# Optimization experiments

Measured on AMD Instinct MI355X. Metric: run time of the kernel, lower is better.

## Reference

```python
import jax, jax.numpy as jnp
import numpy as np

KSIZE = 5      # equivalent steerable kernel size
KMAX = 3       # max circular harmonic
STRIDE = 2
N_IN, N_OUT = 32, 16
B_TOTAL = 3 + 2 * KMAX  # 3 radial atoms at k=0, 2 per harmonic k>=1


def _make_basis():
    # Radial steerable base: Gaussian rings x circular harmonics cos(k*theta)/sin(k*theta)
    ys, xs = np.mgrid[:KSIZE, :KSIZE].astype(np.float64) - (KSIZE - 1) / 2
    r = np.sqrt(xs ** 2 + ys ** 2)
    th = np.arctan2(ys, xs)
    ring = lambda r0: np.exp(-(r - r0) ** 2 / (2 * 0.6 ** 2))
    b0 = np.stack([ring(r0) for r0 in (0.0, 1.0, 2.0)])          # (3, 5, 5)
    br, bi = [], []
    for k in range(1, KMAX + 1):
        br.append(np.stack([ring(r0) * np.cos(k * th) for r0 in (1.0, 2.0)]))  # (2,5,5)
        bi.append(np.stack([ring(r0) * np.sin(k * th) for r0 in (1.0, 2.0)]))
    return (b0.astype(np.float32),
            [b.astype(np.float32) for b in br],
            [b.astype(np.float32) for b in bi])


def _conv_transpose(x, w):
    # torch conv_transpose2d (stride=2, padding='same' -> pad=2, output_padding=1)
    # == dilated-input conv with spatially flipped kernel, explicit pad (2,3).
    rhs = jnp.flip(w, axis=(2, 3))  # (o, i, kh, kw)
    return jax.lax.conv_general_dilated(
        x, rhs, window_strides=(1, 1), padding=((2, 3), (2, 3)),
        lhs_dilation=(STRIDE, STRIDE),
        dimension_numbers=('NCHW', 'OIHW', 'NCHW'))


def setup_inputs() -> dict:
    key = jax.random.key(0)
    k1, k2, k3, k4 = jax.random.split(key, 4)
    x = jax.random.normal(k1, (8, N_IN, 192, 192), jnp.float32)
    # alpha[0]=cos-like, alpha[1]=sin-like field at output resolution; not unit-norm,
    # rho is derived from its norm (rho=None path of forward()).
    alpha = jax.random.normal(k2, (2, 8, 1, 384, 384), jnp.float32)
    weights = jax.random.normal(k3, (N_OUT, N_IN, B_TOTAL), jnp.float32) / np.sqrt(N_IN * B_TOTAL)
    bias = jax.random.normal(k4, (N_OUT,), jnp.float32) * 0.05
    return {"x": x, "alpha": alpha, "weights": weights, "bias": bias}


def reference(x, alpha, weights, bias):
    b0, br, bi = _make_basis()
    # normalize_vector: rho = |alpha|, alpha <- alpha / rho
    rho = jnp.sqrt(jnp.sum(alpha * alpha, axis=0))          # (b, 1, Ho, Wo)
    au = alpha / (rho[None] + 1e-8)
    c1, s1 = au[0], au[1]                                    # cos(a), sin(a)
    # k=0 term (rotation invariant)
    out = _conv_transpose(x, jnp.einsum('oib,bhw->oihw', weights[:, :, :3], jnp.asarray(b0)))
    ck, sk = c1, s1
    off = 3
    for k in range(KMAX):  # harmonics k=1..KMAX, steered by cos(k a), sin(k a)
        wk = weights[:, :, off:off + 2]
        off += 2
        Kr = jnp.einsum('oib,bhw->oihw', wk, jnp.asarray(br[k]))
        Ki = jnp.einsum('oib,bhw->oihw', wk, jnp.asarray(bi[k]))
        out = out + _conv_transpose(x, Kr) * ck + _conv_transpose(x, Ki) * sk
        ckn = ck * c1 - sk * s1  # Chebyshev-style recurrence for cos/sin of (k+1)a
        skn = sk * c1 + ck * s1
        ck, sk = ckn, skn
    return rho * out + bias[None, :, None, None]
```

## Files before the change

### kernel.cpp

```cpp
#include <hip/hip_runtime.h>

#define HIN 192
#define WOUT 384
#define NIN 32
#define NOUT 16
#define NSLOT 9
#define HP 194
#define HPLANE (HP * HP)
#define HQBATCH ((size_t)HPLANE * 18)

typedef float v2f __attribute__((ext_vector_type(2)));

__device__ __forceinline__ unsigned short f2bf(float f) {
    union { float f; unsigned int u; } v; v.f = f;
    unsigned int r = v.u + 0x7fffu + ((v.u >> 16) & 1u);
    return (unsigned short)(r >> 16);
}
__device__ __forceinline__ v2f up2(unsigned u) {
    v2f r;
    r.x = __uint_as_float(u << 16);
    r.y = __uint_as_float(u);
    return r;
}

__global__ __launch_bounds__(256) void kprep_w(const float* __restrict__ w, float* __restrict__ Wt) {
    int t = blockIdx.x * 256 + threadIdx.x;
    if (t >= NIN * NSLOT * NOUT) return;
    int c = t >> 8, r = t & 255;
    int i = r >> 3, j = r & 7;
    int m = c * 8 + j;
    int s = m >> 4, o = m & 15;
    Wt[t] = w[(o * NIN + i) * NSLOT + s];
}

__global__ __launch_bounds__(256) void kzero(uint4* __restrict__ hq, int nb) {
    int t = blockIdx.x * 256 + threadIdx.x;
    if (t >= nb * 772) return;
    int b = t / 772, r = t % 772;
    int iy, ix;
    if (r < 194)      { iy = 0;           ix = r; }
    else if (r < 388) { iy = 193;         ix = r - 194; }
    else if (r < 580) { iy = r - 388 + 1; ix = 0; }
    else              { iy = r - 580 + 1; ix = 193; }
    uint4* p = hq + (size_t)b * HQBATCH + iy * HP + ix;
    uint4 z; z.x = 0; z.y = 0; z.z = 0; z.w = 0;
    #pragma unroll
    for (int c = 0; c < 18; ++c) p[(size_t)c * HPLANE] = z;
}

__global__ __launch_bounds__(256) void kA(const float* __restrict__ x,
                                          const float* __restrict__ Wt,
                                          uint4* __restrict__ hq, int n0) {
    const int b = blockIdx.y;
    const int n = n0 + b;
    const int px = blockIdx.x * 256 + threadIdx.x;
    const int iy = px / HIN, ix = px % HIN;
    const float* xp = x + (size_t)n * NIN * HIN * HIN + px;
    float xv[NIN];
    #pragma unroll
    for (int i = 0; i < NIN; ++i) xv[i] = xp[(size_t)i * HIN * HIN];
    const int pos = (iy + 1) * HP + (ix + 1);
    uint4* hb = hq + (size_t)b * HQBATCH;
    #pragma unroll 1
    for (int c = 0; c < 18; ++c) {
        const float* wc = Wt + c * 256;
        float a[8];
        #pragma unroll
        for (int j = 0; j < 8; ++j) a[j] = 0.0f;
        #pragma unroll
        for (int i = 0; i < NIN; ++i) {
            const float xi = xv[i];
            #pragma unroll
            for (int j = 0; j < 8; ++j) a[j] = fmaf(wc[i * 8 + j], xi, a[j]);
        }
        uint4 v;
        v.x = (unsigned)f2bf(a[0]) | ((unsigned)f2bf(a[1]) << 16);
        v.y = (unsigned)f2bf(a[2]) | ((unsigned)f2bf(a[3]) << 16);
        v.z = (unsigned)f2bf(a[4]) | ((unsigned)f2bf(a[5]) << 16);
        v.w = (unsigned)f2bf(a[6]) | ((unsigned)f2bf(a[7]) << 16);
        hb[(size_t)c * HPLANE + pos] = v;
    }
}

__device__ __forceinline__ void angles(const float* __restrict__ alpha, int n, int oy, int ox,
                                       float (&cc)[3], float (&ss)[3], float& rr) {
    const int aoff = (n * WOUT + oy) * WOUT + ox;
    const float a0 = alpha[aoff];
    const float a1 = alpha[(size_t)8 * WOUT * WOUT + aoff];
    rr = sqrtf(a0 * a0 + a1 * a1);
    const float inv = 1.0f / (rr + 1e-8f);
    cc[0] = a0 * inv;                      ss[0] = a1 * inv;
    cc[1] = cc[0] * cc[0] - ss[0] * ss[0]; ss[1] = 2.0f * cc[0] * ss[0];
    cc[2] = cc[1] * cc[0] - ss[1] * ss[0]; ss[2] = ss[1] * cc[0] + cc[1] * ss[0];
}

__device__ __forceinline__ float ebv(const float2 C, int s,
                                     const float (&cc)[3], const float (&ss)[3]) {
    if (s < 3) return C.x;
    if (s < 5) return C.x * cc[0] + C.y * ss[0];
    if (s < 7) return C.x * cc[1] + C.y * ss[1];
    return C.x * cc[2] + C.y * ss[2];
}

template<int PAIR, int HF>
__device__ __forceinline__ void kb_pair(const uint4* __restrict__ hb,
                                        const float* __restrict__ alpha,
                                        const float* __restrict__ bias_,
                                        float (&stage)[2][16][128],
                                        const float2 (&Cb)[NSLOT][25],
                                        int n, int Y, int X, int lane) {
    constexpr int AX = (PAIR == 0) ? 0 : 1;
    constexpr int BX = (PAIR == 0) ? 1 : 0;

    float ccA[3], ssA[3], ccB[3], ssB[3], rrA, rrB;
    angles(alpha, n, 2 * Y + 0, 2 * X + AX, ccA, ssA, rrA);
    angles(alpha, n, 2 * Y + 1, 2 * X + BX, ccB, ssB, rrB);

    v2f aA[4], aB[4];
    #pragma unroll
    for (int j = 0; j < 4; ++j) { aA[j].x = 0.0f; aA[j].y = 0.0f; aB[j].x = 0.0f; aB[j].y = 0.0f; }

    #pragma unroll 1
    for (int ty = 0; ty < 3; ++ty) {
        const int piy = Y + 2 - ty;
        #pragma unroll 1
        for (int tx = 0; tx < 3; ++tx) {
            const bool useA = (tx < 3 - AX);
            const bool useB = (ty < 2) && (tx < 3 - BX);
            if (!useA && !useB) continue;
            const int pix = X + 2 - tx;
            const unsigned pos = (unsigned)(piy * HP + pix);
            const int biA = (0 + 2 * ty) * 5 + (AX + 2 * tx);
            const int biB = (1 + 2 * ty) * 5 + (BX + 2 * tx);
            if (useA && useB) {
                #pragma unroll
                for (int s = 0; s < NSLOT; ++s) {
                    const uint4 v = hb[(size_t)(2 * s + HF) * HPLANE + pos];
                    const float eA = ebv(Cb[s][biA], s, ccA, ssA);
                    const float eB = ebv(Cb[s][biB], s, ccB, ssB);
                    v2f eA2; eA2.x = eA; eA2.y = eA;
                    v2f eB2; eB2.x = eB; eB2.y = eB;
                    v2f h0 = up2(v.x), h1 = up2(v.y), h2 = up2(v.z), h3 = up2(v.w);
                    aA[0] += eA2 * h0; aA[1] += eA2 * h1; aA[2] += eA2 * h2; aA[3] += eA2 * h3;
                    aB[0] += eB2 * h0; aB[1] += eB2 * h1; aB[2] += eB2 * h2; aB[3] += eB2 * h3;
                }
            } else if (useA) {
                #pragma unroll
                for (int s = 0; s < NSLOT; ++s) {
                    const uint4 v = hb[(size_t)(2 * s + HF) * HPLANE + pos];
                    const float eA = ebv(Cb[s][biA], s, ccA, ssA);
                    v2f eA2; eA2.x = eA; eA2.y = eA;
                    aA[0] += eA2 * up2(v.x); aA[1] += eA2 * up2(v.y);
                    aA[2] += eA2 * up2(v.z); aA[3] += eA2 * up2(v.w);
                }
            } else {
                #pragma unroll
                for (int s = 0; s < NSLOT; ++s) {
                    const uint4 v = hb[(size_t)(2 * s + HF) * HPLANE + pos];
                    const float eB = ebv(Cb[s][biB], s, ccB, ssB);
                    v2f eB2; eB2.x = eB; eB2.y = eB;
                    aB[0] += eB2 * up2(v.x); aB[1] += eB2 * up2(v.y);
                    aB[2] += eB2 * up2(v.z); aB[3] += eB2 * up2(v.w);
                }
            }
        }
    }

    #pragma unroll
    for (int j = 0; j < 4; ++j) {
        stage[0][HF * 8 + 2 * j + 0][2 * lane + AX] = rrA * aA[j].x + bias_[HF * 8 + 2 * j + 0];
        stage[0][HF * 8 + 2 * j + 1][2 * lane + AX] = rrA * aA[j].y + bias_[HF * 8 + 2 * j + 1];
        stage[1][HF * 8 + 2 * j + 0][2 * lane + BX] = rrB * aB[j].x + bias_[HF * 8 + 2 * j + 0];
        stage[1][HF * 8 + 2 * j + 1][2 * lane + BX] = rrB * aB[j].y + bias_[HF * 8 + 2 * j + 1];
    }
}

__global__ __launch_bounds__(256, 4) void kB(const uint4* __restrict__ hq,
                                             const float* __restrict__ alpha,
                                             const float* __restrict__ bias,
                                             float* __restrict__ out, int n0, int nb) {
    __shared__ float2 Cb[NSLOT][25];
    __shared__ float stage[2][16][128];
    {
        const int q = threadIdx.x;
        if (q < NSLOT * 25) {
            int s = q / 25, p = q % 25;
            int ky = p / 5, kx = p % 5;
            float ys = (float)(ky - 2), xs = (float)(kx - 2);
            float r = sqrtf(xs * xs + ys * ys);
            float th = atan2f(ys, xs);
            float cr, ci;
            if (s < 3) {
                float d = r - (float)s;
                cr = expf(-d * d * (1.0f / 0.72f));
                ci = 0.0f;
            } else {
                int k = (s - 3) / 2 + 1;
                float r0 = ((s - 3) & 1) ? 2.0f : 1.0f;
                float d = r - r0;
                float ring = expf(-d * d * (1.0f / 0.72f));
                float a = (float)k * th;
                cr = ring * cosf(a);
                ci = ring * sinf(a);
            }
            Cb[s][p] = make_float2(cr, ci);
        }
    }
    __syncthreads();

    const int tot = gridDim.x;
    const int cpx = tot >> 3;
    const int swz = ((int)blockIdx.x & 7) * cpx + ((int)blockIdx.x >> 3);
    const int Y = swz % 192;
    const int rest = swz / 192;
    const int b = rest % nb;
    const int bx = rest / nb;

    const int n = n0 + b;
    const int lane = threadIdx.x & 63;
    const int wv = threadIdx.x >> 6;
    const int X0 = bx * 64;
    const int X = X0 + lane;
    const uint4* hb = hq + (size_t)b * HQBATCH;

    switch (wv) {
        case 0: kb_pair<0, 0>(hb, alpha, bias, stage, Cb, n, Y, X, lane); break;
        case 1: kb_pair<1, 0>(hb, alpha, bias, stage, Cb, n, Y, X, lane); break;
        case 2: kb_pair<0, 1>(hb, alpha, bias, stage, Cb, n, Y, X, lane); break;
        default: kb_pair<1, 1>(hb, alpha, bias, stage, Cb, n, Y, X, lane); break;
    }

    __syncthreads();

    #pragma unroll
    for (int q = 0; q < 16; ++q) {
        const int f = q * 256 + threadIdx.x;
        const int row = f >> 7, col = f & 127;
        const int py = row >> 4, o = row & 15;
        out[(((size_t)n * NOUT + o) * WOUT + (2 * Y + py)) * WOUT + 2 * X0 + col]
            = stage[py][o][col];
    }
}

__global__ __launch_bounds__(256) void steered_convT(
    const float* __restrict__ x, const float* __restrict__ alpha,
    const float* __restrict__ weights, const float* __restrict__ bias,
    float* __restrict__ out) {
    __shared__ float sb[15 * 25];
    for (int q = threadIdx.x; q < 375; q += 256) {
        int s = q / 25, p = q % 25;
        int ky = p / 5, kx = p % 5;
        float ys = (float)(ky - 2), xs = (float)(kx - 2);
        float r = sqrtf(xs * xs + ys * ys);
        float th = atan2f(ys, xs);
        float val;
        if (s < 3) { float d = r - (float)s; val = expf(-d * d * (1.0f / 0.72f)); }
        else {
            int k = (s - 3) / 4 + 1; int rem = (s - 3) & 3;
            float r0 = (rem & 1) ? 2.0f : 1.0f; float d = r - r0;
            float ring = expf(-d * d * (1.0f / 0.72f));
            float ang = (float)k * th;
            val = ring * ((rem < 2) ? cosf(ang) : sinf(ang));
        }
        sb[q] = val;
    }
    __syncthreads();
    int idx = blockIdx.x * 256 + threadIdx.x;
    int ox = idx % WOUT; int tt = idx / WOUT; int oy = tt % WOUT; int n = tt / WOUT;
    const int plane = WOUT * WOUT;
    int aoff = (n * WOUT + oy) * WOUT + ox;
    float a0 = alpha[aoff], a1 = alpha[8 * plane + aoff];
    float rho = sqrtf(a0 * a0 + a1 * a1);
    float inv = 1.0f / (rho + 1e-8f);
    float c1 = a0 * inv, s1 = a1 * inv;
    float c2 = c1 * c1 - s1 * s1, s2 = 2.0f * s1 * c1;
    float c3 = c2 * c1 - s2 * s1, s3 = s2 * c1 + c2 * s1;
    int py = oy & 1, px = ox & 1;
    int iy0 = (oy >> 1) + 1, ix0 = (ox >> 1) + 1;
    float eb[9][9]; int off[9];
    #pragma unroll
    for (int t = 0; t < 9; ++t) {
        int ty = t / 3, tx = t % 3;
        int ky = py + 2 * ty, kx = px + 2 * tx;
        int iy = iy0 - ty, ix = ix0 - tx;
        bool v = (ky < 5) && (kx < 5) && (iy >= 0) && (iy < HIN) && (ix >= 0) && (ix < HIN);
        float m = v ? 1.0f : 0.0f;
        int ciy = min(max(iy, 0), HIN - 1), cix = min(max(ix, 0), HIN - 1);
        off[t] = ciy * HIN + cix;
        int bi_ = min(ky, 4) * 5 + min(kx, 4);
        eb[0][t] = sb[0 * 25 + bi_] * m;
        eb[1][t] = sb[1 * 25 + bi_] * m;
        eb[2][t] = sb[2 * 25 + bi_] * m;
        eb[3][t] = (sb[3 * 25 + bi_] * c1 + sb[5 * 25 + bi_] * s1) * m;
        eb[4][t] = (sb[4 * 25 + bi_] * c1 + sb[6 * 25 + bi_] * s1) * m;
        eb[5][t] = (sb[7 * 25 + bi_] * c2 + sb[9 * 25 + bi_] * s2) * m;
        eb[6][t] = (sb[8 * 25 + bi_] * c2 + sb[10 * 25 + bi_] * s2) * m;
        eb[7][t] = (sb[11 * 25 + bi_] * c3 + sb[13 * 25 + bi_] * s3) * m;
        eb[8][t] = (sb[12 * 25 + bi_] * c3 + sb[14 * 25 + bi_] * s3) * m;
    }
    float acc[NOUT];
    #pragma unroll
    for (int o = 0; o < NOUT; ++o) acc[o] = 0.0f;
    const float* xn = x + (size_t)n * NIN * HIN * HIN;
    for (int i = 0; i < NIN; ++i) {
        const float* xp = xn + (size_t)i * HIN * HIN;
        float tap[9];
        #pragma unroll
        for (int t = 0; t < 9; ++t) tap[t] = xp[off[t]];
        float G[9];
        #pragma unroll
        for (int b = 0; b < 9; ++b) {
            float s = 0.0f;
            #pragma unroll
            for (int t = 0; t < 9; ++t) s += eb[b][t] * tap[t];
            G[b] = s;
        }
        const float* wp = weights + i * 9;
        #pragma unroll
        for (int o = 0; o < NOUT; ++o) {
            float s = acc[o];
            #pragma unroll
            for (int b = 0; b < 9; ++b) s += wp[o * NIN * 9 + b] * G[b];
            acc[o] = s;
        }
    }
    #pragma unroll
    for (int o = 0; o < NOUT; ++o)
        out[((size_t)(n * NOUT + o) * WOUT + oy) * WOUT + ox] = rho * acc[o] + bias[o];
}

extern "C" void kernel_launch(void* const* d_in, const int* in_sizes, int n_in,
                              void* d_out, int out_size, void* d_ws, size_t ws_size,
                              hipStream_t stream) {
    const float* x       = (const float*)d_in[0];
    const float* alpha   = (const float*)d_in[1];
    const float* weights = (const float*)d_in[2];
    const float* bias    = (const float*)d_in[3];
    float* out = (float*)d_out;

    const size_t hoff = 32768;
    const size_t perb = HQBATCH * 16;
    int cb = 0;
    if (ws_size > hoff) cb = (int)((ws_size - hoff) / perb);
    if (cb > 8) cb = 8;

    if (cb < 1) {
        const int pixels = 8 * WOUT * WOUT;
        steered_convT<<<dim3(pixels / 256), 256, 0, stream>>>(x, alpha, weights, bias, out);
        return;
    }

    float* Wt = (float*)d_ws;
    uint4* hq = (uint4*)((char*)d_ws + hoff);

    kprep_w<<<dim3(18), 256, 0, stream>>>(weights, Wt);

    for (int n0 = 0; n0 < 8; n0 += cb) {
        int nb = 8 - n0; if (nb > cb) nb = cb;
        kzero<<<dim3((nb * 772 + 255) / 256), 256, 0, stream>>>(hq, nb);
        kA<<<dim3(144, nb), 256, 0, stream>>>(x, Wt, hq, n0);
        kB<<<dim3(576 * nb), 256, 0, stream>>>(hq, alpha, bias, out, n0, nb);
    }
}
```

Baseline: 139.0 us.

## Have each wave compute all four output phases to reuse loaded hq values

Restructures kB so each wave handles all four sub-pixel output phases (quad) of one half of the output channels, instead of two waves each handling a pair of phases. Each loaded bf16 hq vector is now reused across up to four accumulators, which halves the redundant global loads of the intermediate. The block shrinks from 256 to 128 threads and the copy-out loop doubles its iterations. Register pressure rises (16 v2f accumulators plus 4 sets of angles), which may reduce occupancy, and the basis-setup loop now strides by 128.

```diff
diff --git a/kernel.cpp b/kernel.cpp
--- a/kernel.cpp
+++ b/kernel.cpp
@@ -102,80 +102,103 @@
     return C.x * cc[2] + C.y * ss[2];
 }
 
-template<int PAIR, int HF>
-__device__ __forceinline__ void kb_pair(const uint4* __restrict__ hb,
+template<int HF>
+__device__ __forceinline__ void kb_quad(const uint4* __restrict__ hb,
                                         const float* __restrict__ alpha,
                                         const float* __restrict__ bias_,
                                         float (&stage)[2][16][128],
                                         const float2 (&Cb)[NSLOT][25],
                                         int n, int Y, int X, int lane) {
-    constexpr int AX = (PAIR == 0) ? 0 : 1;
-    constexpr int BX = (PAIR == 0) ? 1 : 0;
-
-    float ccA[3], ssA[3], ccB[3], ssB[3], rrA, rrB;
-    angles(alpha, n, 2 * Y + 0, 2 * X + AX, ccA, ssA, rrA);
-    angles(alpha, n, 2 * Y + 1, 2 * X + BX, ccB, ssB, rrB);
-
-    v2f aA[4], aB[4];
-    #pragma unroll
-    for (int j = 0; j < 4; ++j) { aA[j].x = 0.0f; aA[j].y = 0.0f; aB[j].x = 0.0f; aB[j].y = 0.0f; }
+    float cc[4][3], ss[4][3], rr[4];
+    #pragma unroll
+    for (int p = 0; p < 4; ++p)
+        angles(alpha, n, 2 * Y + (p >> 1), 2 * X + (p & 1), cc[p], ss[p], rr[p]);
+
+    v2f acc[4][4];
+    #pragma unroll
+    for (int p = 0; p < 4; ++p)
+        #pragma unroll
+        for (int j = 0; j < 4; ++j) { acc[p][j].x = 0.0f; acc[p][j].y = 0.0f; }
 
     #pragma unroll 1
     for (int ty = 0; ty < 3; ++ty) {
         const int piy = Y + 2 - ty;
+        const bool tyok = (ty < 2);
         #pragma unroll 1
         for (int tx = 0; tx < 3; ++tx) {
-            const bool useA = (tx < 3 - AX);
-            const bool useB = (ty < 2) && (tx < 3 - BX);
-            if (!useA && !useB) continue;
-            const int pix = X + 2 - tx;
-            const unsigned pos = (unsigned)(piy * HP + pix);
-            const int biA = (0 + 2 * ty) * 5 + (AX + 2 * tx);
-            const int biB = (1 + 2 * ty) * 5 + (BX + 2 * tx);
-            if (useA && useB) {
+            const bool txok = (tx < 2);
+            const unsigned pos = (unsigned)(piy * HP + (X + 2 - tx));
+            const int b00 = (2 * ty) * 5 + (2 * tx);
+            if (tyok && txok) {
                 #pragma unroll
                 for (int s = 0; s < NSLOT; ++s) {
                     const uint4 v = hb[(size_t)(2 * s + HF) * HPLANE + pos];
-                    const float eA = ebv(Cb[s][biA], s, ccA, ssA);
-                    const float eB = ebv(Cb[s][biB], s, ccB, ssB);
-                    v2f eA2; eA2.x = eA; eA2.y = eA;
-                    v2f eB2; eB2.x = eB; eB2.y = eB;
-                    v2f h0 = up2(v.x), h1 = up2(v.y), h2 = up2(v.z), h3 = up2(v.w);
-                    aA[0] += eA2 * h0; aA[1] += eA2 * h1; aA[2] += eA2 * h2; aA[3] += eA2 * h3;
-                    aB[0] += eB2 * h0; aB[1] += eB2 * h1; aB[2] += eB2 * h2; aB[3] += eB2 * h3;
+                    const v2f h0 = up2(v.x), h1 = up2(v.y), h2 = up2(v.z), h3 = up2(v.w);
+                    const float e0 = ebv(Cb[s][b00],     s, cc[0], ss[0]);
+                    const float e1 = ebv(Cb[s][b00 + 1], s, cc[1], ss[1]);
+                    const float e2 = ebv(Cb[s][b00 + 5], s, cc[2], ss[2]);
+                    const float e3 = ebv(Cb[s][b00 + 6], s, cc[3], ss[3]);
+                    v2f e;
+                    e.x = e0; e.y = e0;
+                    acc[0][0] += e * h0; acc[0][1] += e * h1; acc[0][2] += e * h2; acc[0][3] += e * h3;
+                    e.x = e1; e.y = e1;
+                    acc[1][0] += e * h0; acc[1][1] += e * h1; acc[1][2] += e * h2; acc[1][3] += e * h3;
+                    e.x = e2; e.y = e2;
+                    acc[2][0] += e * h0; acc[2][1] += e * h1; acc[2][2] += e * h2; acc[2][3] += e * h3;
+                    e.x = e3; e.y = e3;
+                    acc[3][0] += e * h0; acc[3][1] += e * h1; acc[3][2] += e * h2; acc[3][3] += e * h3;
                 }
-            } else if (useA) {
+            } else if (tyok) {
                 #pragma unroll
                 for (int s = 0; s < NSLOT; ++s) {
                     const uint4 v = hb[(size_t)(2 * s + HF) * HPLANE + pos];
-                    const float eA = ebv(Cb[s][biA], s, ccA, ssA);
-                    v2f eA2; eA2.x = eA; eA2.y = eA;
-                    aA[0] += eA2 * up2(v.x); aA[1] += eA2 * up2(v.y);
-                    aA[2] += eA2 * up2(v.z); aA[3] += eA2 * up2(v.w);
+                    const v2f h0 = up2(v.x), h1 = up2(v.y), h2 = up2(v.z), h3 = up2(v.w);
+                    const float e0 = ebv(Cb[s][b00],     s, cc[0], ss[0]);
+                    const float e2 = ebv(Cb[s][b00 + 5], s, cc[2], ss[2]);
+                    v2f e;
+                    e.x = e0; e.y = e0;
+                    acc[0][0] += e * h0; acc[0][1] += e * h1; acc[0][2] += e * h2; acc[0][3] += e * h3;
+                    e.x = e2; e.y = e2;
+                    acc[2][0] += e * h0; acc[2][1] += e * h1; acc[2][2] += e * h2; acc[2][3] += e * h3;
+                }
+            } else if (txok) {
+                #pragma unroll
+                for (int s = 0; s < NSLOT; ++s) {
+                    const uint4 v = hb[(size_t)(2 * s + HF) * HPLANE + pos];
+                    const v2f h0 = up2(v.x), h1 = up2(v.y), h2 = up2(v.z), h3 = up2(v.w);
+                    const float e0 = ebv(Cb[s][b00],     s, cc[0], ss[0]);
+                    const float e1 = ebv(Cb[s][b00 + 1], s, cc[1], ss[1]);
+                    v2f e;
+                    e.x = e0; e.y = e0;
+                    acc[0][0] += e * h0; acc[0][1] += e * h1; acc[0][2] += e * h2; acc[0][3] += e * h3;
+                    e.x = e1; e.y = e1;
+                    acc[1][0] += e * h0; acc[1][1] += e * h1; acc[1][2] += e * h2; acc[1][3] += e * h3;
                 }
             } else {
                 #pragma unroll
                 for (int s = 0; s < NSLOT; ++s) {
                     const uint4 v = hb[(size_t)(2 * s + HF) * HPLANE + pos];
-                    const float eB = ebv(Cb[s][biB], s, ccB, ssB);
-                    v2f eB2; eB2.x = eB; eB2.y = eB;
-                    aB[0] += eB2 * up2(v.x); aB[1] += eB2 * up2(v.y);
-                    aB[2] += eB2 * up2(v.z); aB[3] += eB2 * up2(v.w);
+                    const float e0 = ebv(Cb[s][b00], s, cc[0], ss[0]);
+                    v2f e; e.x = e0; e.y = e0;
+                    acc[0][0] += e * up2(v.x); acc[0][1] += e * up2(v.y);
+                    acc[0][2] += e * up2(v.z); acc[0][3] += e * up2(v.w);
                 }
             }
         }
     }
 
     #pragma unroll
-    for (int j = 0; j < 4; ++j) {
-        stage[0][HF * 8 + 2 * j + 0][2 * lane + AX] = rrA * aA[j].x + bias_[HF * 8 + 2 * j + 0];
-        stage[0][HF * 8 + 2 * j + 1][2 * lane + AX] = rrA * aA[j].y + bias_[HF * 8 + 2 * j + 1];
-        stage[1][HF * 8 + 2 * j + 0][2 * lane + BX] = rrB * aB[j].x + bias_[HF * 8 + 2 * j + 0];
-        stage[1][HF * 8 + 2 * j + 1][2 * lane + BX] = rrB * aB[j].y + bias_[HF * 8 + 2 * j + 1];
-    }
-}
-
-__global__ __launch_bounds__(256, 4) void kB(const uint4* __restrict__ hq,
+    for (int p = 0; p < 4; ++p) {
+        const int py = p >> 1, px = p & 1;
+        #pragma unroll
+        for (int j = 0; j < 4; ++j) {
+            stage[py][HF * 8 + 2 * j + 0][2 * lane + px] = rr[p] * acc[p][j].x + bias_[HF * 8 + 2 * j + 0];
+            stage[py][HF * 8 + 2 * j + 1][2 * lane + px] = rr[p] * acc[p][j].y + bias_[HF * 8 + 2 * j + 1];
+        }
+    }
+}
+
+__global__ __launch_bounds__(128, 4) void kB(const uint4* __restrict__ hq,
                                              const float* __restrict__ alpha,
                                              const float* __restrict__ bias,
                                              float* __restrict__ out, int n0, int nb) {
@@ -183,8 +206,9 @@
     __shared__ float stage[2][16][128];
     {
         const int q = threadIdx.x;
-        if (q < NSLOT * 25) {
-            int s = q / 25, p = q % 25;
+        if (q < 128 && q < NSLOT * 25) {  }
+        for (int qq = threadIdx.x; qq < NSLOT * 25; qq += 128) {
+            int s = qq / 25, p = qq % 25;
             int ky = p / 5, kx = p % 5;
             float ys = (float)(ky - 2), xs = (float)(kx - 2);
             float r = sqrtf(xs * xs + ys * ys);
@@ -223,18 +247,14 @@
     const int X = X0 + lane;
     const uint4* hb = hq + (size_t)b * HQBATCH;
 
-    switch (wv) {
-        case 0: kb_pair<0, 0>(hb, alpha, bias, stage, Cb, n, Y, X, lane); break;
-        case 1: kb_pair<1, 0>(hb, alpha, bias, stage, Cb, n, Y, X, lane); break;
-        case 2: kb_pair<0, 1>(hb, alpha, bias, stage, Cb, n, Y, X, lane); break;
-        default: kb_pair<1, 1>(hb, alpha, bias, stage, Cb, n, Y, X, lane); break;
-    }
+    if (wv == 0) kb_quad<0>(hb, alpha, bias, stage, Cb, n, Y, X, lane);
+    else         kb_quad<1>(hb, alpha, bias, stage, Cb, n, Y, X, lane);
 
     __syncthreads();
 
     #pragma unroll
-    for (int q = 0; q < 16; ++q) {
-        const int f = q * 256 + threadIdx.x;
+    for (int q = 0; q < 32; ++q) {
+        const int f = q * 128 + threadIdx.x;
         const int row = f >> 7, col = f & 127;
         const int py = row >> 4, o = row & 15;
         out[(((size_t)n * NOUT + o) * WOUT + (2 * Y + py)) * WOUT + 2 * X0 + col]
@@ -359,6 +379,6 @@
         int nb = 8 - n0; if (nb > cb) nb = cb;
         kzero<<<dim3((nb * 772 + 255) / 256), 256, 0, stream>>>(hq, nb);
         kA<<<dim3(144, nb), 256, 0, stream>>>(x, Wt, hq, n0);
-        kB<<<dim3(576 * nb), 256, 0, stream>>>(hq, alpha, bias, out, n0, nb);
-    }
-}
+        kB<<<dim3(576 * nb), 128, 0, stream>>>(hq, alpha, bias, out, n0, nb);
+    }
+}
```

Measured after the change: 144.5 us. 3.9% more time.
